# Optimization experiments

Hardware: AMD Instinct MI355X
Metric: run time of the kernel (lower is better)

Reference implementation:

```python
import jax, jax.numpy as jnp
import numpy as np

B, S, L, D, C_ENC, H = 8, 4096, 77, 1280, 2048, 20
DH = D // H          # 64
SCALE = DH ** -0.5


def setup_inputs() -> dict:
    key = jax.random.key(0)
    ks = jax.random.split(key, 8)
    return {
        "hidden_states": jax.random.normal(ks[0], (B, S, D), jnp.float32),
        "encoder_hidden_states": jax.random.normal(ks[1], (B, L, C_ENC), jnp.float32),
        "region_state": jax.random.uniform(ks[2], (B, S, L), jnp.float32),
        "Wq": jax.random.normal(ks[3], (D, D), jnp.float32) * 0.02,
        "Wk": jax.random.normal(ks[4], (C_ENC, D), jnp.float32) * 0.02,
        "Wv": jax.random.normal(ks[5], (C_ENC, D), jnp.float32) * 0.02,
        "Wo": jax.random.normal(ks[6], (D, D), jnp.float32) * 0.02,
        "bo": jnp.zeros((D,), jnp.float32),
        "sigma": jnp.ones((1,), jnp.float32) * 14.6,
    }


def reference(hidden_states, encoder_hidden_states, region_state, Wq, Wk, Wv, Wo, bo, sigma):
    # QKV projections (dense GEMMs)
    q = (hidden_states @ Wq).reshape(B, S, H, DH)            # [B,S,H,dh]
    k = (encoder_hidden_states @ Wk).reshape(B, L, H, DH)    # [B,L,H,dh]
    v = (encoder_hidden_states @ Wv).reshape(B, L, H, DH)
    # scaled attention scores (baddbmm with beta=0 == plain scaled matmul)
    scores = jnp.einsum('bshd,blhd->bhsl', q, k) * SCALE      # [B,H,S,L]
    # region-prompt bias: weight_func(w, sigma, qk) = w * log(1 + 0.1*sigma) * qk.max()
    # repeat_interleave over heads == broadcast over the head axis
    bias = region_state * (jnp.log1p(sigma[0] * 0.1) * scores.max())  # [B,S,L]
    scores = scores + bias[:, None, :, :]
    probs = jax.nn.softmax(scores, axis=-1)
    out = jnp.einsum('bhsl,blhd->bshd', probs, v).reshape(B, S, D)
    # output projection (to_out[0]); to_out[1] is dropout (identity at eval)
    return out @ Wo + bo
```

## Files before the change

### kernel.cpp

```cpp
#include <hip/hip_runtime.h>
#include <hip/hip_bf16.h>
#include <math.h>

#define NB 8
#define NS 4096
#define NL 77
#define NLP 80
#define NLPV 96
#define ND 1280
#define NC 2048
#define NH 20
#define NDH 64
#define QK_SCALE 0.125f

typedef __attribute__((ext_vector_type(4))) float f32x4;
typedef __attribute__((ext_vector_type(8))) short bf16x8;

static __device__ __forceinline__ void gload_lds16(const void* g, void* l) {
  __builtin_amdgcn_global_load_lds(
      (const __attribute__((address_space(1))) void*)g,
      (__attribute__((address_space(3))) void*)l, 16, 0, 0);
}

#define BAR() do { asm volatile("" ::: "memory"); __builtin_amdgcn_s_barrier(); asm volatile("" ::: "memory"); } while (0)
#define LGKM0() asm volatile("s_waitcnt lgkmcnt(0)" ::: "memory")

__global__ void cvt_bf16_kern(const float* __restrict__ in,
                              __hip_bfloat16* __restrict__ out, long n)
{
  long i = ((long)blockIdx.x * blockDim.x + threadIdx.x) * 4;
  long stride = (long)gridDim.x * blockDim.x * 4;
  for (; i < n; i += stride) {
    float4 v = *reinterpret_cast<const float4*>(in + i);
    union { __hip_bfloat16 h[4]; ushort4 u; } r;
    r.h[0] = __float2bfloat16(v.x);
    r.h[1] = __float2bfloat16(v.y);
    r.h[2] = __float2bfloat16(v.z);
    r.h[3] = __float2bfloat16(v.w);
    *reinterpret_cast<ushort4*>(out + i) = r.u;
  }
}

__global__ void transpose_bf16_kern(const float* __restrict__ in,
                                    __hip_bfloat16* __restrict__ out,
                                    int rows, int cols)
{
  __shared__ float t[32][33];
  int c0 = blockIdx.x * 32, r0 = blockIdx.y * 32;
  int tx = threadIdx.x, ty = threadIdx.y;
  for (int i = ty; i < 32; i += 8) {
    int r = r0 + i, c = c0 + tx;
    t[i][tx] = (r < rows && c < cols) ? in[(long)r * cols + c] : 0.f;
  }
  __syncthreads();
  for (int i = ty; i < 32; i += 8) {
    int oc = c0 + i, orr = r0 + tx;
    if (oc < cols && orr < rows)
      out[(long)oc * rows + orr] = __float2bfloat16(t[tx][i]);
  }
}

__global__ __launch_bounds__(256)
void gemm_bt_kern(const __hip_bfloat16* __restrict__ A,
                  const __hip_bfloat16* __restrict__ Bt,
                  void* __restrict__ C, const float* __restrict__ bias,
                  int M, int N, int K, int mode)
{
  __shared__ __align__(16) __hip_bfloat16 As[128 * 32];
  __shared__ __align__(16) __hip_bfloat16 Bs[128 * 32];
  const int t = threadIdx.x;
  const int lane = t & 63;
  const int w = t >> 6;
  const int wm = w >> 1, wn = w & 1;
  const int lr = lane & 15, hi = lane >> 4, lk = hi * 8;
  const long m0 = (long)blockIdx.x * 128;
  const long n0 = (long)blockIdx.y * 128;

  f32x4 acc[4][4];
#pragma unroll
  for (int mi = 0; mi < 4; ++mi)
#pragma unroll
    for (int ni = 0; ni < 4; ++ni) acc[mi][ni] = {0.f, 0.f, 0.f, 0.f};

  for (int k0 = 0; k0 < K; k0 += 32) {
    __syncthreads();
#pragma unroll
    for (int rnd = 0; rnd < 2; ++rnd) {
      int idx = rnd * 256 + t;
      int row = idx >> 2, kpp = (idx & 3) * 8;
      long arow = m0 + row; if (arow >= M) arow = M - 1;
      gload_lds16(A + arow * K + k0 + kpp, (void*)(As + idx * 8));
      long brow = n0 + row;
      gload_lds16(Bt + brow * K + k0 + kpp, (void*)(Bs + idx * 8));
    }
    __syncthreads();

    bf16x8 af[4], bfr[4];
#pragma unroll
    for (int i = 0; i < 4; ++i) {
      af[i]  = *reinterpret_cast<const bf16x8*>(As + (wm * 64 + i * 16 + lr) * 32 + lk);
      bfr[i] = *reinterpret_cast<const bf16x8*>(Bs + (wn * 64 + i * 16 + lr) * 32 + lk);
    }
#pragma unroll
    for (int mi = 0; mi < 4; ++mi)
#pragma unroll
      for (int ni = 0; ni < 4; ++ni)
        acc[mi][ni] = __builtin_amdgcn_mfma_f32_16x16x32_bf16(af[mi], bfr[ni], acc[mi][ni], 0, 0, 0);
  }

#pragma unroll
  for (int mi = 0; mi < 4; ++mi) {
#pragma unroll
    for (int r = 0; r < 4; ++r) {
      long row = m0 + wm * 64 + mi * 16 + hi * 4 + r;
      if (row < M) {
#pragma unroll
        for (int ni = 0; ni < 4; ++ni) {
          long col = n0 + wn * 64 + ni * 16 + lr;
          if (mode == 0)
            ((__hip_bfloat16*)C)[row * N + col] = __float2bfloat16(acc[mi][ni][r]);
          else
            ((float*)C)[row * N + col] = acc[mi][ni][r] + bias[col];
        }
      }
    }
  }
}

__global__ __launch_bounds__(512, 1)
void gemm256_kern(const __hip_bfloat16* __restrict__ A,
                  const __hip_bfloat16* __restrict__ Bt,
                  void* __restrict__ C, const float* __restrict__ bias,
                  int M, int N, int K, int mode)
{
  __shared__ __align__(16) __hip_bfloat16 sm[65536];
  char* smc = (char*)sm;

  const int t = threadIdx.x, lane = t & 63, w = t >> 6;
  const int wm = w >> 2, wn = w & 3;
  const int lr = lane & 15, hi = lane >> 4;

  int nwg = gridDim.x;
  int cpx = nwg >> 3;
  int swz = (blockIdx.x & 7) * cpx + (blockIdx.x >> 3);
  int nxt = N >> 8;
  int mt = swz / nxt, ntile = swz - mt * nxt;
  const long m0 = (long)mt * 256, n0 = (long)ntile * 256;

  const int rA   = w * 16 + (lane >> 3);
  const int sg8  = (((lane & 7) ^ (lane >> 3))) * 8;
  const int dst0 = (w * 128 + lane) * 8;

  const int swz16 = (hi * 16) ^ ((lr & 7) << 4);
  const int aoff0 = (wm * 128 + lr) * 128 + swz16;
  const int boff0 = (wn * 64 + lr) * 128 + swz16;

  f32x4 acc[8][4];
#pragma unroll
  for (int j = 0; j < 8; ++j)
#pragma unroll
    for (int ni = 0; ni < 4; ++ni) acc[j][ni] = {0.f, 0.f, 0.f, 0.f};

  bf16x8 af[4][2], bfr[4][2];

  auto stageA = [&](int b, int h, int kt) {
#pragma unroll
    for (int c = 0; c < 2; ++c)
      gload_lds16(A + (m0 + h * 128 + rA + c * 8) * (long)K + kt * 64 + sg8,
                  (void*)(sm + b * 16384 + h * 8192 + dst0 + c * 512));
  };
  auto stageB = [&](int b, int h, int kt) {
#pragma unroll
    for (int c = 0; c < 2; ++c)
      gload_lds16(Bt + (n0 + h * 128 + rA + c * 8) * (long)K + kt * 64 + sg8,
                  (void*)(sm + 32768 + b * 16384 + h * 8192 + dst0 + c * 512));
  };

  const int NT = K >> 6;
  stageB(0, 0, 0); stageB(0, 1, 0); stageA(0, 0, 0); stageA(0, 1, 0);
  stageB(1, 0, 1); stageB(1, 1, 1); stageA(1, 0, 1); stageA(1, 1, 1);
  asm volatile("s_waitcnt vmcnt(8)" ::: "memory");
  BAR();

  for (int t2 = 0; t2 < NT; ++t2) {
    const int b = t2 & 1;
    const char* pa = smc + b * 32768;
    const char* pb = smc + 65536 + b * 32768;
    const bool pf = (t2 + 2 < NT);

#pragma unroll
    for (int mi = 0; mi < 4; ++mi) {
      af[mi][0] = *reinterpret_cast<const bf16x8*>(pa + (aoff0 + mi * 2048));
      af[mi][1] = *reinterpret_cast<const bf16x8*>(pa + ((aoff0 ^ 64) + mi * 2048));
    }
#pragma unroll
    for (int ni = 0; ni < 2; ++ni) {
      bfr[ni][0] = *reinterpret_cast<const bf16x8*>(pb + (boff0 + ni * 2048));
      bfr[ni][1] = *reinterpret_cast<const bf16x8*>(pb + ((boff0 ^ 64) + ni * 2048));
    }
    BAR();
    LGKM0();
    __builtin_amdgcn_s_setprio(1);
#pragma unroll
    for (int mi = 0; mi < 4; ++mi)
#pragma unroll
      for (int ni = 0; ni < 2; ++ni) {
        acc[mi][ni] = __builtin_amdgcn_mfma_f32_16x16x32_bf16(af[mi][0], bfr[ni][0], acc[mi][ni], 0, 0, 0);
        acc[mi][ni] = __builtin_amdgcn_mfma_f32_16x16x32_bf16(af[mi][1], bfr[ni][1], acc[mi][ni], 0, 0, 0);
      }
    __builtin_amdgcn_s_setprio(0);
    BAR();

#pragma unroll
    for (int ni = 2; ni < 4; ++ni) {
      bfr[ni][0] = *reinterpret_cast<const bf16x8*>(pb + (boff0 + ni * 2048));
      bfr[ni][1] = *reinterpret_cast<const bf16x8*>(pb + ((boff0 ^ 64) + ni * 2048));
    }
    BAR();
    LGKM0();
    __builtin_amdgcn_s_setprio(1);
#pragma unroll
    for (int mi = 0; mi < 4; ++mi)
#pragma unroll
      for (int ni = 2; ni < 4; ++ni) {
        acc[mi][ni] = __builtin_amdgcn_mfma_f32_16x16x32_bf16(af[mi][0], bfr[ni][0], acc[mi][ni], 0, 0, 0);
        acc[mi][ni] = __builtin_amdgcn_mfma_f32_16x16x32_bf16(af[mi][1], bfr[ni][1], acc[mi][ni], 0, 0, 0);
      }
    __builtin_amdgcn_s_setprio(0);
    BAR();

#pragma unroll
    for (int mi = 0; mi < 4; ++mi) {
      af[mi][0] = *reinterpret_cast<const bf16x8*>(pa + (aoff0 + 8192 + mi * 2048));
      af[mi][1] = *reinterpret_cast<const bf16x8*>(pa + ((aoff0 ^ 64) + 8192 + mi * 2048));
    }
    if (pf) { stageB(b, 0, t2 + 2); stageB(b, 1, t2 + 2); }
    BAR();
    LGKM0();
    __builtin_amdgcn_s_setprio(1);
#pragma unroll
    for (int mi = 0; mi < 4; ++mi)
#pragma unroll
      for (int ni = 2; ni < 4; ++ni) {
        acc[mi + 4][ni] = __builtin_amdgcn_mfma_f32_16x16x32_bf16(af[mi][0], bfr[ni][0], acc[mi + 4][ni], 0, 0, 0);
        acc[mi + 4][ni] = __builtin_amdgcn_mfma_f32_16x16x32_bf16(af[mi][1], bfr[ni][1], acc[mi + 4][ni], 0, 0, 0);
      }
    __builtin_amdgcn_s_setprio(0);
    BAR();

    if (pf) { stageA(b, 0, t2 + 2); stageA(b, 1, t2 + 2); }
    BAR();
    __builtin_amdgcn_s_setprio(1);
#pragma unroll
    for (int mi = 0; mi < 4; ++mi)
#pragma unroll
      for (int ni = 0; ni < 2; ++ni) {
        acc[mi + 4][ni] = __builtin_amdgcn_mfma_f32_16x16x32_bf16(af[mi][0], bfr[ni][0], acc[mi + 4][ni], 0, 0, 0);
        acc[mi + 4][ni] = __builtin_amdgcn_mfma_f32_16x16x32_bf16(af[mi][1], bfr[ni][1], acc[mi + 4][ni], 0, 0, 0);
      }
    __builtin_amdgcn_s_setprio(0);
    if (pf) { asm volatile("s_waitcnt vmcnt(8)" ::: "memory"); }
    else    { asm volatile("s_waitcnt vmcnt(0)" ::: "memory"); }
    BAR();
  }

#pragma unroll
  for (int j = 0; j < 8; ++j) {
#pragma unroll
    for (int r = 0; r < 4; ++r) {
      long row = m0 + wm * 128 + j * 16 + hi * 4 + r;
#pragma unroll
      for (int ni = 0; ni < 4; ++ni) {
        long col = n0 + wn * 64 + ni * 16 + lr;
        if (mode == 0)
          ((__hip_bfloat16*)C)[row * N + col] = __float2bfloat16(acc[j][ni][r]);
        else
          ((float*)C)[row * N + col] = acc[j][ni][r] + bias[col];
      }
    }
  }
}

__global__ void repack_kv_kern(const __hip_bfloat16* __restrict__ kvc,
                               __hip_bfloat16* __restrict__ kp,
                               __hip_bfloat16* __restrict__ vt)
{
  int idx = blockIdx.x * 256 + threadIdx.x;
  const __hip_bfloat16 z = __float2bfloat16(0.f);
  if (idx < NB * NLP * ND) {
    int d = idx % ND;
    int l = (idx / ND) % NLP;
    int b = idx / (ND * NLP);
    kp[idx] = (l < NL) ? kvc[((long)(b * NL + l)) * 2560 + d] : z;
  }
  if (idx < NB * NH * NDH * NLPV) {
    int l  = idx % NLPV;
    int dh = (idx / NLPV) % NDH;
    int h  = (idx / (NLPV * NDH)) % NH;
    int b  = idx / (NLPV * NDH * NH);
    vt[idx] = (l < NL) ? kvc[((long)(b * NL + l)) * 2560 + ND + h * NDH + dh] : z;
  }
}

__global__ __launch_bounds__(256)
void qk_max_kern(const __hip_bfloat16* __restrict__ qb,
                 const __hip_bfloat16* __restrict__ kp,
                 float* __restrict__ bmax)
{
  int t = threadIdx.x, lane = t & 63, wi = t >> 6;
  int b = blockIdx.z, h = blockIdx.y;
  int s0 = blockIdx.x * 64 + wi * 16;
  int lr = lane & 15, lk = (lane >> 4) * 8;

  const __hip_bfloat16* Qp = qb + ((long)(b * NS + s0 + lr)) * ND + h * NDH + lk;
  bf16x8 aq0 = *reinterpret_cast<const bf16x8*>(Qp);
  bf16x8 aq1 = *reinterpret_cast<const bf16x8*>(Qp + 32);

  float m = -1e30f;
#pragma unroll
  for (int lt = 0; lt < 5; ++lt) {
    const __hip_bfloat16* Kr = kp + ((long)(b * NLP + lt * 16 + lr)) * ND + h * NDH + lk;
    bf16x8 bk0 = *reinterpret_cast<const bf16x8*>(Kr);
    bf16x8 bk1 = *reinterpret_cast<const bf16x8*>(Kr + 32);
    f32x4 sc = {0.f, 0.f, 0.f, 0.f};
    sc = __builtin_amdgcn_mfma_f32_16x16x32_bf16(aq0, bk0, sc, 0, 0, 0);
    sc = __builtin_amdgcn_mfma_f32_16x16x32_bf16(aq1, bk1, sc, 0, 0, 0);
    bool valid = (lt < 4) || (lr < 13);
    if (valid) {
#pragma unroll
      for (int r = 0; r < 4; ++r) m = fmaxf(m, sc[r]);
    }
  }
#pragma unroll
  for (int k = 32; k >= 1; k >>= 1) m = fmaxf(m, __shfl_xor(m, k));

  __shared__ float wmx[4];
  if (lane == 0) wmx[wi] = m;
  __syncthreads();
  if (t == 0) {
    float mm = fmaxf(fmaxf(wmx[0], wmx[1]), fmaxf(wmx[2], wmx[3]));
    long bid = ((long)blockIdx.z * gridDim.y + blockIdx.y) * gridDim.x + blockIdx.x;
    bmax[bid] = mm * QK_SCALE;
  }
}

__global__ void reduce_max_kern(const float* __restrict__ bm, int n,
                                const float* __restrict__ sigma,
                                float* __restrict__ cb)
{
  __shared__ float sm[256];
  float m = -1e30f;
  for (int i = threadIdx.x; i < n; i += 256) m = fmaxf(m, bm[i]);
  sm[threadIdx.x] = m;
  __syncthreads();
  for (int s = 128; s > 0; s >>= 1) {
    if (threadIdx.x < (unsigned)s) sm[threadIdx.x] = fmaxf(sm[threadIdx.x], sm[threadIdx.x + s]);
    __syncthreads();
  }
  if (threadIdx.x == 0) cb[0] = log1pf(sigma[0] * 0.1f) * sm[0];
}

__global__ __launch_bounds__(256)
void attn_kern(const __hip_bfloat16* __restrict__ qb,
               const __hip_bfloat16* __restrict__ kp,
               const __hip_bfloat16* __restrict__ vt,
               const float* __restrict__ rs,
               const float* __restrict__ cb,
               __hip_bfloat16* __restrict__ ao_out)
{
  __shared__ __align__(16) __hip_bfloat16 pl[4][16][NLPV];
  int t = threadIdx.x, lane = t & 63, wi = t >> 6;
  int b = blockIdx.z, h = blockIdx.y;
  int s0 = blockIdx.x * 64 + wi * 16;
  int lr = lane & 15, hi = lane >> 4, lk = hi * 8;
  const float c = cb[0];

  const __hip_bfloat16* Qp = qb + ((long)(b * NS + s0 + lr)) * ND + h * NDH + lk;
  bf16x8 aq0 = *reinterpret_cast<const bf16x8*>(Qp);
  bf16x8 aq1 = *reinterpret_cast<const bf16x8*>(Qp + 32);

  f32x4 sc[5];
#pragma unroll
  for (int lt = 0; lt < 5; ++lt) {
    const __hip_bfloat16* Kr = kp + ((long)(b * NLP + lt * 16 + lr)) * ND + h * NDH + lk;
    bf16x8 bk0 = *reinterpret_cast<const bf16x8*>(Kr);
    bf16x8 bk1 = *reinterpret_cast<const bf16x8*>(Kr + 32);
    f32x4 z = {0.f, 0.f, 0.f, 0.f};
    z = __builtin_amdgcn_mfma_f32_16x16x32_bf16(aq0, bk0, z, 0, 0, 0);
    sc[lt] = __builtin_amdgcn_mfma_f32_16x16x32_bf16(aq1, bk1, z, 0, 0, 0);
  }

  float sv[5][4];
  float pm[4] = {-1e30f, -1e30f, -1e30f, -1e30f};
#pragma unroll
  for (int lt = 0; lt < 5; ++lt) {
    int l = lt * 16 + lr;
#pragma unroll
    for (int r = 0; r < 4; ++r) {
      if (l < NL) {
        int srow = s0 + hi * 4 + r;
        float v = sc[lt][r] * QK_SCALE + rs[((long)(b * NS + srow)) * NL + l] * c;
        sv[lt][r] = v;
        pm[r] = fmaxf(pm[r], v);
      } else {
        sv[lt][r] = -1e30f;
      }
    }
  }
#pragma unroll
  for (int r = 0; r < 4; ++r)
#pragma unroll
    for (int k = 8; k >= 1; k >>= 1) pm[r] = fmaxf(pm[r], __shfl_xor(pm[r], k));

  float p[5][4];
  float psum[4] = {0.f, 0.f, 0.f, 0.f};
#pragma unroll
  for (int lt = 0; lt < 5; ++lt) {
    int l = lt * 16 + lr;
#pragma unroll
    for (int r = 0; r < 4; ++r) {
      float e = (l < NL) ? __expf(sv[lt][r] - pm[r]) : 0.f;
      p[lt][r] = e;
      psum[r] += e;
    }
  }
#pragma unroll
  for (int r = 0; r < 4; ++r)
#pragma unroll
    for (int k = 8; k >= 1; k >>= 1) psum[r] += __shfl_xor(psum[r], k);
  float rinv[4];
#pragma unroll
  for (int r = 0; r < 4; ++r) rinv[r] = 1.f / psum[r];

#pragma unroll
  for (int lt = 0; lt < 5; ++lt)
#pragma unroll
    for (int r = 0; r < 4; ++r)
      pl[wi][hi * 4 + r][lt * 16 + lr] = __float2bfloat16(p[lt][r]);
#pragma unroll
  for (int r = 0; r < 4; ++r)
    pl[wi][hi * 4 + r][80 + lr] = __float2bfloat16(0.f);

  f32x4 ao[4];
#pragma unroll
  for (int nt = 0; nt < 4; ++nt) ao[nt] = {0.f, 0.f, 0.f, 0.f};
  const __hip_bfloat16* Vb = vt + ((long)((b * NH + h) * NDH)) * NLPV;
#pragma unroll
  for (int ks = 0; ks < 3; ++ks) {
    bf16x8 pa = *reinterpret_cast<const bf16x8*>(&pl[wi][lr][ks * 32 + lk]);
#pragma unroll
    for (int nt = 0; nt < 4; ++nt) {
      bf16x8 bv = *reinterpret_cast<const bf16x8*>(Vb + ((long)(nt * 16 + lr)) * NLPV + ks * 32 + lk);
      ao[nt] = __builtin_amdgcn_mfma_f32_16x16x32_bf16(pa, bv, ao[nt], 0, 0, 0);
    }
  }

#pragma unroll
  for (int nt = 0; nt < 4; ++nt)
#pragma unroll
    for (int r = 0; r < 4; ++r) {
      int srow = s0 + hi * 4 + r;
      ao_out[((long)(b * NS + srow)) * ND + h * NDH + nt * 16 + lr] =
          __float2bfloat16(ao[nt][r] * rinv[r]);
    }
}

extern "C" void kernel_launch(void* const* d_in, const int* in_sizes, int n_in,
                              void* d_out, int out_size, void* d_ws, size_t ws_size,
                              hipStream_t stream)
{
  const float* hs    = (const float*)d_in[0];
  const float* ehs   = (const float*)d_in[1];
  const float* rs    = (const float*)d_in[2];
  const float* Wq    = (const float*)d_in[3];
  const float* Wk    = (const float*)d_in[4];
  const float* Wv    = (const float*)d_in[5];
  const float* Wo    = (const float*)d_in[6];
  const float* bo    = (const float*)d_in[7];
  const float* sigma = (const float*)d_in[8];
  float* out = (float*)d_out;

  char* ws = (char*)d_ws;
  size_t off = 0;
  auto alloc = [&](size_t bytes) {
    void* p = ws + off;
    off = (off + bytes + 255) & ~(size_t)255;
    return p;
  };
  __hip_bfloat16* hsb  = (__hip_bfloat16*)alloc((size_t)NB * NS * ND * 2);
  __hip_bfloat16* qb   = (__hip_bfloat16*)alloc((size_t)NB * NS * ND * 2);
  __hip_bfloat16* wqt  = (__hip_bfloat16*)alloc((size_t)ND * ND * 2);
  __hip_bfloat16* wkvt = (__hip_bfloat16*)alloc((size_t)2560 * NC * 2);
  __hip_bfloat16* wot  = (__hip_bfloat16*)alloc((size_t)ND * ND * 2);
  __hip_bfloat16* ehsb = (__hip_bfloat16*)alloc((size_t)NB * NL * NC * 2);
  __hip_bfloat16* kvc  = (__hip_bfloat16*)alloc((size_t)NB * NL * 2560 * 2);
  __hip_bfloat16* kp   = (__hip_bfloat16*)alloc((size_t)NB * NLP * ND * 2);
  __hip_bfloat16* vt   = (__hip_bfloat16*)alloc((size_t)NB * NH * NDH * NLPV * 2);
  float* bmax = (float*)alloc(10240 * 4);
  float* cb   = (float*)alloc(256);

  cvt_bf16_kern<<<2048, 256, 0, stream>>>(hs, hsb, (long)NB * NS * ND);
  cvt_bf16_kern<<<512, 256, 0, stream>>>(ehs, ehsb, (long)NB * NL * NC);

  transpose_bf16_kern<<<dim3(40, 40), dim3(32, 8), 0, stream>>>(Wq, wqt, ND, ND);
  transpose_bf16_kern<<<dim3(40, 64), dim3(32, 8), 0, stream>>>(Wk, wkvt, NC, ND);
  transpose_bf16_kern<<<dim3(40, 64), dim3(32, 8), 0, stream>>>(Wv, wkvt + (size_t)ND * NC, NC, ND);
  transpose_bf16_kern<<<dim3(40, 40), dim3(32, 8), 0, stream>>>(Wo, wot, ND, ND);

  gemm256_kern<<<640, 512, 0, stream>>>(hsb, wqt, qb, nullptr, NB * NS, ND, ND, 0);

  gemm_bt_kern<<<dim3(5, 20), 256, 0, stream>>>(ehsb, wkvt, kvc, nullptr, NB * NL, 2560, NC, 0);

  repack_kv_kern<<<3840, 256, 0, stream>>>(kvc, kp, vt);

  qk_max_kern<<<dim3(64, NH, NB), 256, 0, stream>>>(qb, kp, bmax);
  reduce_max_kern<<<1, 256, 0, stream>>>(bmax, 64 * NH * NB, sigma, cb);

  attn_kern<<<dim3(64, NH, NB), 256, 0, stream>>>(qb, kp, vt, rs, cb, hsb);

  gemm256_kern<<<640, 512, 0, stream>>>(hsb, wot, out, bo, NB * NS, ND, ND, 1);
}
```

Baseline: 581.2 us.

## Collapse GEMM main-loop barriers and stage epilogue stores through LDS

The GEMM main loop drops most intra-iteration barriers and lgkmcnt waits. It loads all four B fragments at once and issues both the A and B prefetch stages together after a single barrier. The epilogue now writes each 16-row accumulator slab into a per-wave LDS scratch area, then emits 16-byte coalesced global stores instead of scattered scalar stores. Fewer barriers should improve MFMA issue density. The risks are more register pressure, since all B fragments stay live, and LDS races: scratch and prefetch writes may overlap buffers that other waves are still reading without a barrier.

```diff
diff --git a/kernel.cpp b/kernel.cpp
--- a/kernel.cpp
+++ b/kernel.cpp
@@ -23,7 +23,6 @@
 }
 
 #define BAR() do { asm volatile("" ::: "memory"); __builtin_amdgcn_s_barrier(); asm volatile("" ::: "memory"); } while (0)
-#define LGKM0() asm volatile("s_waitcnt lgkmcnt(0)" ::: "memory")
 
 __global__ void cvt_bf16_kern(const float* __restrict__ in,
                               __hip_bfloat16* __restrict__ out, long n)
@@ -194,49 +193,25 @@
       af[mi][1] = *reinterpret_cast<const bf16x8*>(pa + ((aoff0 ^ 64) + mi * 2048));
     }
 #pragma unroll
-    for (int ni = 0; ni < 2; ++ni) {
+    for (int ni = 0; ni < 4; ++ni) {
       bfr[ni][0] = *reinterpret_cast<const bf16x8*>(pb + (boff0 + ni * 2048));
       bfr[ni][1] = *reinterpret_cast<const bf16x8*>(pb + ((boff0 ^ 64) + ni * 2048));
     }
-    BAR();
-    LGKM0();
     __builtin_amdgcn_s_setprio(1);
 #pragma unroll
     for (int mi = 0; mi < 4; ++mi)
 #pragma unroll
-      for (int ni = 0; ni < 2; ++ni) {
+      for (int ni = 0; ni < 4; ++ni) {
         acc[mi][ni] = __builtin_amdgcn_mfma_f32_16x16x32_bf16(af[mi][0], bfr[ni][0], acc[mi][ni], 0, 0, 0);
         acc[mi][ni] = __builtin_amdgcn_mfma_f32_16x16x32_bf16(af[mi][1], bfr[ni][1], acc[mi][ni], 0, 0, 0);
       }
     __builtin_amdgcn_s_setprio(0);
-    BAR();
-
-#pragma unroll
-    for (int ni = 2; ni < 4; ++ni) {
-      bfr[ni][0] = *reinterpret_cast<const bf16x8*>(pb + (boff0 + ni * 2048));
-      bfr[ni][1] = *reinterpret_cast<const bf16x8*>(pb + ((boff0 ^ 64) + ni * 2048));
-    }
-    BAR();
-    LGKM0();
-    __builtin_amdgcn_s_setprio(1);
-#pragma unroll
-    for (int mi = 0; mi < 4; ++mi)
-#pragma unroll
-      for (int ni = 2; ni < 4; ++ni) {
-        acc[mi][ni] = __builtin_amdgcn_mfma_f32_16x16x32_bf16(af[mi][0], bfr[ni][0], acc[mi][ni], 0, 0, 0);
-        acc[mi][ni] = __builtin_amdgcn_mfma_f32_16x16x32_bf16(af[mi][1], bfr[ni][1], acc[mi][ni], 0, 0, 0);
-      }
-    __builtin_amdgcn_s_setprio(0);
-    BAR();
 
 #pragma unroll
     for (int mi = 0; mi < 4; ++mi) {
       af[mi][0] = *reinterpret_cast<const bf16x8*>(pa + (aoff0 + 8192 + mi * 2048));
       af[mi][1] = *reinterpret_cast<const bf16x8*>(pa + ((aoff0 ^ 64) + 8192 + mi * 2048));
     }
-    if (pf) { stageB(b, 0, t2 + 2); stageB(b, 1, t2 + 2); }
-    BAR();
-    LGKM0();
     __builtin_amdgcn_s_setprio(1);
 #pragma unroll
     for (int mi = 0; mi < 4; ++mi)
@@ -246,10 +221,11 @@
         acc[mi + 4][ni] = __builtin_amdgcn_mfma_f32_16x16x32_bf16(af[mi][1], bfr[ni][1], acc[mi + 4][ni], 0, 0, 0);
       }
     __builtin_amdgcn_s_setprio(0);
+
     BAR();
-
-    if (pf) { stageA(b, 0, t2 + 2); stageA(b, 1, t2 + 2); }
-    BAR();
+    if (pf) { stageB(b, 0, t2 + 2); stageB(b, 1, t2 + 2);
+              stageA(b, 0, t2 + 2); stageA(b, 1, t2 + 2); }
+
     __builtin_amdgcn_s_setprio(1);
 #pragma unroll
     for (int mi = 0; mi < 4; ++mi)
@@ -259,23 +235,54 @@
         acc[mi + 4][ni] = __builtin_amdgcn_mfma_f32_16x16x32_bf16(af[mi][1], bfr[ni][1], acc[mi + 4][ni], 0, 0, 0);
       }
     __builtin_amdgcn_s_setprio(0);
+
     if (pf) { asm volatile("s_waitcnt vmcnt(8)" ::: "memory"); }
     else    { asm volatile("s_waitcnt vmcnt(0)" ::: "memory"); }
     BAR();
   }
 
-#pragma unroll
-  for (int j = 0; j < 8; ++j) {
-#pragma unroll
-    for (int r = 0; r < 4; ++r) {
-      long row = m0 + wm * 128 + j * 16 + hi * 4 + r;
-#pragma unroll
-      for (int ni = 0; ni < 4; ++ni) {
-        long col = n0 + wn * 64 + ni * 16 + lr;
-        if (mode == 0)
-          ((__hip_bfloat16*)C)[row * N + col] = __float2bfloat16(acc[j][ni][r]);
-        else
-          ((float*)C)[row * N + col] = acc[j][ni][r] + bias[col];
+  char* wsc = smc + w * 4096;
+  if (mode == 0) {
+    __hip_bfloat16* wsb = (__hip_bfloat16*)wsc;
+#pragma unroll
+    for (int j = 0; j < 8; ++j) {
+#pragma unroll
+      for (int ni = 0; ni < 4; ++ni)
+#pragma unroll
+        for (int r = 0; r < 4; ++r)
+          wsb[(hi * 4 + r) * 64 + ni * 16 + lr] = __float2bfloat16(acc[j][ni][r]);
+      asm volatile("s_waitcnt lgkmcnt(0)" ::: "memory");
+#pragma unroll
+      for (int c = 0; c < 2; ++c) {
+        int chunk = c * 64 + lane;
+        int row = chunk >> 3, col8 = chunk & 7;
+        int4 v = *reinterpret_cast<const int4*>(wsc + chunk * 16);
+        long grow = m0 + wm * 128 + j * 16 + row;
+        long gcol = n0 + wn * 64 + col8 * 8;
+        *reinterpret_cast<int4*>((__hip_bfloat16*)C + grow * N + gcol) = v;
+      }
+    }
+  } else {
+    float bv[4];
+#pragma unroll
+    for (int ni = 0; ni < 4; ++ni) bv[ni] = bias[n0 + wn * 64 + ni * 16 + lr];
+    float* wsf = (float*)wsc;
+#pragma unroll
+    for (int j = 0; j < 8; ++j) {
+#pragma unroll
+      for (int ni = 0; ni < 4; ++ni)
+#pragma unroll
+        for (int r = 0; r < 4; ++r)
+          wsf[(hi * 4 + r) * 64 + ni * 16 + lr] = acc[j][ni][r] + bv[ni];
+      asm volatile("s_waitcnt lgkmcnt(0)" ::: "memory");
+#pragma unroll
+      for (int c = 0; c < 4; ++c) {
+        int chunk = c * 64 + lane;
+        int row = chunk >> 4, col4 = chunk & 15;
+        int4 v = *reinterpret_cast<const int4*>(wsc + chunk * 16);
+        long grow = m0 + wm * 128 + j * 16 + row;
+        long gcol = n0 + wn * 64 + col4 * 4;
+        *reinterpret_cast<int4*>((float*)C + grow * N + gcol) = v;
       }
     }
   }
```

Measured after the change: 540.4 us. 1.08x faster.

## Use 128x128 GEMM tiles and process four query tiles per attention wave

Applied to the files above, without the earlier changes.

Swaps the 256x256, 512-thread GEMM for a 128x128, 256-thread kernel with two blocks per CU and a simpler single-phase MFMA loop per k-step. The QK-max and attention kernels now load each head's K fragments into registers once per wave and loop over four 16-row query tiles, cutting their grids by four. The aim is better occupancy and load balance for the large GEMMs and less redundant K loading in attention. The trade-off is lower per-tile data reuse in the GEMM and higher register pressure in the attention kernels.

```diff
diff --git a/kernel.cpp b/kernel.cpp
--- a/kernel.cpp
+++ b/kernel.cpp
@@ -127,157 +127,124 @@
   }
 }
 
-__global__ __launch_bounds__(512, 1)
-void gemm256_kern(const __hip_bfloat16* __restrict__ A,
+__global__ __launch_bounds__(256, 2)
+void gemm128_kern(const __hip_bfloat16* __restrict__ A,
                   const __hip_bfloat16* __restrict__ Bt,
                   void* __restrict__ C, const float* __restrict__ bias,
                   int M, int N, int K, int mode)
 {
-  __shared__ __align__(16) __hip_bfloat16 sm[65536];
+  __shared__ __align__(16) __hip_bfloat16 sm[32768];
   char* smc = (char*)sm;
 
   const int t = threadIdx.x, lane = t & 63, w = t >> 6;
-  const int wm = w >> 2, wn = w & 3;
+  const int wm = w >> 1, wn = w & 1;
   const int lr = lane & 15, hi = lane >> 4;
+  const int sw = lr & 7;
 
   int nwg = gridDim.x;
   int cpx = nwg >> 3;
   int swz = (blockIdx.x & 7) * cpx + (blockIdx.x >> 3);
-  int nxt = N >> 8;
+  int nxt = N >> 7;
   int mt = swz / nxt, ntile = swz - mt * nxt;
-  const long m0 = (long)mt * 256, n0 = (long)ntile * 256;
-
-  const int rA   = w * 16 + (lane >> 3);
-  const int sg8  = (((lane & 7) ^ (lane >> 3))) * 8;
-  const int dst0 = (w * 128 + lane) * 8;
-
-  const int swz16 = (hi * 16) ^ ((lr & 7) << 4);
-  const int aoff0 = (wm * 128 + lr) * 128 + swz16;
-  const int boff0 = (wn * 64 + lr) * 128 + swz16;
-
-  f32x4 acc[8][4];
-#pragma unroll
-  for (int j = 0; j < 8; ++j)
-#pragma unroll
-    for (int ni = 0; ni < 4; ++ni) acc[j][ni] = {0.f, 0.f, 0.f, 0.f};
-
-  bf16x8 af[4][2], bfr[4][2];
-
-  auto stageA = [&](int b, int h, int kt) {
-#pragma unroll
-    for (int c = 0; c < 2; ++c)
-      gload_lds16(A + (m0 + h * 128 + rA + c * 8) * (long)K + kt * 64 + sg8,
-                  (void*)(sm + b * 16384 + h * 8192 + dst0 + c * 512));
+  const long m0 = (long)mt * 128, n0 = (long)ntile * 128;
+
+  const int srow  = t >> 3;
+  const int skoff = ((t & 7) ^ (srow & 7)) * 8;
+  const int sdst  = t * 16;
+
+  f32x4 acc[4][4];
+#pragma unroll
+  for (int mi = 0; mi < 4; ++mi)
+#pragma unroll
+    for (int ni = 0; ni < 4; ++ni) acc[mi][ni] = {0.f, 0.f, 0.f, 0.f};
+
+  auto stageA = [&](int b, int kt) {
+#pragma unroll
+    for (int c = 0; c < 4; ++c)
+      gload_lds16(A + (m0 + c * 32 + srow) * (long)K + kt * 64 + skoff,
+                  (void*)(smc + b * 16384 + c * 4096 + sdst));
   };
-  auto stageB = [&](int b, int h, int kt) {
-#pragma unroll
-    for (int c = 0; c < 2; ++c)
-      gload_lds16(Bt + (n0 + h * 128 + rA + c * 8) * (long)K + kt * 64 + sg8,
-                  (void*)(sm + 32768 + b * 16384 + h * 8192 + dst0 + c * 512));
+  auto stageB = [&](int b, int kt) {
+#pragma unroll
+    for (int c = 0; c < 4; ++c)
+      gload_lds16(Bt + (n0 + c * 32 + srow) * (long)K + kt * 64 + skoff,
+                  (void*)(smc + 32768 + b * 16384 + c * 4096 + sdst));
   };
 
   const int NT = K >> 6;
-  stageB(0, 0, 0); stageB(0, 1, 0); stageA(0, 0, 0); stageA(0, 1, 0);
-  stageB(1, 0, 1); stageB(1, 1, 1); stageA(1, 0, 1); stageA(1, 1, 1);
+  stageA(0, 0); stageB(0, 0);
+  stageA(1, 1); stageB(1, 1);
   asm volatile("s_waitcnt vmcnt(8)" ::: "memory");
   BAR();
 
   for (int t2 = 0; t2 < NT; ++t2) {
     const int b = t2 & 1;
-    const char* pa = smc + b * 32768;
-    const char* pb = smc + 65536 + b * 32768;
+    const char* pa = smc + b * 16384;
+    const char* pb = smc + 32768 + b * 16384;
     const bool pf = (t2 + 2 < NT);
 
+    bf16x8 af[4][2], bfr[4][2];
 #pragma unroll
     for (int mi = 0; mi < 4; ++mi) {
-      af[mi][0] = *reinterpret_cast<const bf16x8*>(pa + (aoff0 + mi * 2048));
-      af[mi][1] = *reinterpret_cast<const bf16x8*>(pa + ((aoff0 ^ 64) + mi * 2048));
-    }
-#pragma unroll
-    for (int ni = 0; ni < 2; ++ni) {
-      bfr[ni][0] = *reinterpret_cast<const bf16x8*>(pb + (boff0 + ni * 2048));
-      bfr[ni][1] = *reinterpret_cast<const bf16x8*>(pb + ((boff0 ^ 64) + ni * 2048));
-    }
-    BAR();
-    LGKM0();
+      int row = wm * 64 + mi * 16 + lr;
+#pragma unroll
+      for (int kk = 0; kk < 2; ++kk)
+        af[mi][kk] = *reinterpret_cast<const bf16x8*>(
+            pa + row * 128 + ((((kk * 4 + hi) ^ sw)) << 4));
+    }
+#pragma unroll
+    for (int ni = 0; ni < 4; ++ni) {
+      int row = wn * 64 + ni * 16 + lr;
+#pragma unroll
+      for (int kk = 0; kk < 2; ++kk)
+        bfr[ni][kk] = *reinterpret_cast<const bf16x8*>(
+            pb + row * 128 + ((((kk * 4 + hi) ^ sw)) << 4));
+    }
     __builtin_amdgcn_s_setprio(1);
 #pragma unroll
     for (int mi = 0; mi < 4; ++mi)
 #pragma unroll
-      for (int ni = 0; ni < 2; ++ni) {
+      for (int ni = 0; ni < 4; ++ni) {
         acc[mi][ni] = __builtin_amdgcn_mfma_f32_16x16x32_bf16(af[mi][0], bfr[ni][0], acc[mi][ni], 0, 0, 0);
         acc[mi][ni] = __builtin_amdgcn_mfma_f32_16x16x32_bf16(af[mi][1], bfr[ni][1], acc[mi][ni], 0, 0, 0);
       }
     __builtin_amdgcn_s_setprio(0);
+
+    LGKM0();
     BAR();
-
-#pragma unroll
-    for (int ni = 2; ni < 4; ++ni) {
-      bfr[ni][0] = *reinterpret_cast<const bf16x8*>(pb + (boff0 + ni * 2048));
-      bfr[ni][1] = *reinterpret_cast<const bf16x8*>(pb + ((boff0 ^ 64) + ni * 2048));
-    }
-    BAR();
-    LGKM0();
-    __builtin_amdgcn_s_setprio(1);
-#pragma unroll
-    for (int mi = 0; mi < 4; ++mi)
-#pragma unroll
-      for (int ni = 2; ni < 4; ++ni) {
-        acc[mi][ni] = __builtin_amdgcn_mfma_f32_16x16x32_bf16(af[mi][0], bfr[ni][0], acc[mi][ni], 0, 0, 0);
-        acc[mi][ni] = __builtin_amdgcn_mfma_f32_16x16x32_bf16(af[mi][1], bfr[ni][1], acc[mi][ni], 0, 0, 0);
-      }
-    __builtin_amdgcn_s_setprio(0);
-    BAR();
-
-#pragma unroll
-    for (int mi = 0; mi < 4; ++mi) {
-      af[mi][0] = *reinterpret_cast<const bf16x8*>(pa + (aoff0 + 8192 + mi * 2048));
-      af[mi][1] = *reinterpret_cast<const bf16x8*>(pa + ((aoff0 ^ 64) + 8192 + mi * 2048));
-    }
-    if (pf) { stageB(b, 0, t2 + 2); stageB(b, 1, t2 + 2); }
-    BAR();
-    LGKM0();
-    __builtin_amdgcn_s_setprio(1);
-#pragma unroll
-    for (int mi = 0; mi < 4; ++mi)
-#pragma unroll
-      for (int ni = 2; ni < 4; ++ni) {
-        acc[mi + 4][ni] = __builtin_amdgcn_mfma_f32_16x16x32_bf16(af[mi][0], bfr[ni][0], acc[mi + 4][ni], 0, 0, 0);
-        acc[mi + 4][ni] = __builtin_amdgcn_mfma_f32_16x16x32_bf16(af[mi][1], bfr[ni][1], acc[mi + 4][ni], 0, 0, 0);
-      }
-    __builtin_amdgcn_s_setprio(0);
-    BAR();
-
-    if (pf) { stageA(b, 0, t2 + 2); stageA(b, 1, t2 + 2); }
-    BAR();
-    __builtin_amdgcn_s_setprio(1);
-#pragma unroll
-    for (int mi = 0; mi < 4; ++mi)
-#pragma unroll
-      for (int ni = 0; ni < 2; ++ni) {
-        acc[mi + 4][ni] = __builtin_amdgcn_mfma_f32_16x16x32_bf16(af[mi][0], bfr[ni][0], acc[mi + 4][ni], 0, 0, 0);
-        acc[mi + 4][ni] = __builtin_amdgcn_mfma_f32_16x16x32_bf16(af[mi][1], bfr[ni][1], acc[mi + 4][ni], 0, 0, 0);
-      }
-    __builtin_amdgcn_s_setprio(0);
+    if (pf) { stageA(b, t2 + 2); stageB(b, t2 + 2); }
     if (pf) { asm volatile("s_waitcnt vmcnt(8)" ::: "memory"); }
     else    { asm volatile("s_waitcnt vmcnt(0)" ::: "memory"); }
     BAR();
   }
 
-#pragma unroll
-  for (int j = 0; j < 8; ++j) {
-#pragma unroll
-    for (int r = 0; r < 4; ++r) {
-      long row = m0 + wm * 128 + j * 16 + hi * 4 + r;
-#pragma unroll
-      for (int ni = 0; ni < 4; ++ni) {
-        long col = n0 + wn * 64 + ni * 16 + lr;
-        if (mode == 0)
-          ((__hip_bfloat16*)C)[row * N + col] = __float2bfloat16(acc[j][ni][r]);
-        else
-          ((float*)C)[row * N + col] = acc[j][ni][r] + bias[col];
-      }
-    }
+  if (mode == 0) {
+#pragma unroll
+    for (int mi = 0; mi < 4; ++mi)
+#pragma unroll
+      for (int r = 0; r < 4; ++r) {
+        long row = m0 + wm * 64 + mi * 16 + hi * 4 + r;
+#pragma unroll
+        for (int ni = 0; ni < 4; ++ni) {
+          long col = n0 + wn * 64 + ni * 16 + lr;
+          ((__hip_bfloat16*)C)[row * N + col] = __float2bfloat16(acc[mi][ni][r]);
+        }
+      }
+  } else {
+    float bv[4];
+#pragma unroll
+    for (int ni = 0; ni < 4; ++ni) bv[ni] = bias[n0 + wn * 64 + ni * 16 + lr];
+#pragma unroll
+    for (int mi = 0; mi < 4; ++mi)
+#pragma unroll
+      for (int r = 0; r < 4; ++r) {
+        long row = m0 + wm * 64 + mi * 16 + hi * 4 + r;
+#pragma unroll
+        for (int ni = 0; ni < 4; ++ni) {
+          long col = n0 + wn * 64 + ni * 16 + lr;
+          ((float*)C)[row * N + col] = acc[mi][ni][r] + bv[ni];
+        }
+      }
   }
 }
 
@@ -309,26 +276,33 @@
 {
   int t = threadIdx.x, lane = t & 63, wi = t >> 6;
   int b = blockIdx.z, h = blockIdx.y;
-  int s0 = blockIdx.x * 64 + wi * 16;
   int lr = lane & 15, lk = (lane >> 4) * 8;
 
-  const __hip_bfloat16* Qp = qb + ((long)(b * NS + s0 + lr)) * ND + h * NDH + lk;
-  bf16x8 aq0 = *reinterpret_cast<const bf16x8*>(Qp);
-  bf16x8 aq1 = *reinterpret_cast<const bf16x8*>(Qp + 32);
-
-  float m = -1e30f;
+  bf16x8 bk[5][2];
 #pragma unroll
   for (int lt = 0; lt < 5; ++lt) {
     const __hip_bfloat16* Kr = kp + ((long)(b * NLP + lt * 16 + lr)) * ND + h * NDH + lk;
-    bf16x8 bk0 = *reinterpret_cast<const bf16x8*>(Kr);
-    bf16x8 bk1 = *reinterpret_cast<const bf16x8*>(Kr + 32);
-    f32x4 sc = {0.f, 0.f, 0.f, 0.f};
-    sc = __builtin_amdgcn_mfma_f32_16x16x32_bf16(aq0, bk0, sc, 0, 0, 0);
-    sc = __builtin_amdgcn_mfma_f32_16x16x32_bf16(aq1, bk1, sc, 0, 0, 0);
-    bool valid = (lt < 4) || (lr < 13);
-    if (valid) {
-#pragma unroll
-      for (int r = 0; r < 4; ++r) m = fmaxf(m, sc[r]);
+    bk[lt][0] = *reinterpret_cast<const bf16x8*>(Kr);
+    bk[lt][1] = *reinterpret_cast<const bf16x8*>(Kr + 32);
+  }
+
+  float m = -1e30f;
+#pragma unroll
+  for (int st = 0; st < 4; ++st) {
+    int s0 = blockIdx.x * 256 + wi * 64 + st * 16;
+    const __hip_bfloat16* Qp = qb + ((long)(b * NS + s0 + lr)) * ND + h * NDH + lk;
+    bf16x8 aq0 = *reinterpret_cast<const bf16x8*>(Qp);
+    bf16x8 aq1 = *reinterpret_cast<const bf16x8*>(Qp + 32);
+#pragma unroll
+    for (int lt = 0; lt < 5; ++lt) {
+      f32x4 sc = {0.f, 0.f, 0.f, 0.f};
+      sc = __builtin_amdgcn_mfma_f32_16x16x32_bf16(aq0, bk[lt][0], sc, 0, 0, 0);
+      sc = __builtin_amdgcn_mfma_f32_16x16x32_bf16(aq1, bk[lt][1], sc, 0, 0, 0);
+      bool valid = (lt < 4) || (lr < 13);
+      if (valid) {
+#pragma unroll
+        for (int r = 0; r < 4; ++r) m = fmaxf(m, sc[r]);
+      }
     }
   }
 #pragma unroll
@@ -371,98 +345,111 @@
   __shared__ __align__(16) __hip_bfloat16 pl[4][16][NLPV];
   int t = threadIdx.x, lane = t & 63, wi = t >> 6;
   int b = blockIdx.z, h = blockIdx.y;
-  int s0 = blockIdx.x * 64 + wi * 16;
   int lr = lane & 15, hi = lane >> 4, lk = hi * 8;
   const float c = cb[0];
 
-  const __hip_bfloat16* Qp = qb + ((long)(b * NS + s0 + lr)) * ND + h * NDH + lk;
-  bf16x8 aq0 = *reinterpret_cast<const bf16x8*>(Qp);
-  bf16x8 aq1 = *reinterpret_cast<const bf16x8*>(Qp + 32);
-
-  f32x4 sc[5];
+  bf16x8 bk[5][2];
 #pragma unroll
   for (int lt = 0; lt < 5; ++lt) {
     const __hip_bfloat16* Kr = kp + ((long)(b * NLP + lt * 16 + lr)) * ND + h * NDH + lk;
-    bf16x8 bk0 = *reinterpret_cast<const bf16x8*>(Kr);
-    bf16x8 bk1 = *reinterpret_cast<const bf16x8*>(Kr + 32);
-    f32x4 z = {0.f, 0.f, 0.f, 0.f};
-    z = __builtin_amdgcn_mfma_f32_16x16x32_bf16(aq0, bk0, z, 0, 0, 0);
-    sc[lt] = __builtin_amdgcn_mfma_f32_16x16x32_bf16(aq1, bk1, z, 0, 0, 0);
-  }
-
-  float sv[5][4];
-  float pm[4] = {-1e30f, -1e30f, -1e30f, -1e30f};
-#pragma unroll
-  for (int lt = 0; lt < 5; ++lt) {
-    int l = lt * 16 + lr;
-#pragma unroll
-    for (int r = 0; r < 4; ++r) {
-      if (l < NL) {
-        int srow = s0 + hi * 4 + r;
-        float v = sc[lt][r] * QK_SCALE + rs[((long)(b * NS + srow)) * NL + l] * c;
-        sv[lt][r] = v;
-        pm[r] = fmaxf(pm[r], v);
-      } else {
-        sv[lt][r] = -1e30f;
-      }
-    }
-  }
-#pragma unroll
-  for (int r = 0; r < 4; ++r)
-#pragma unroll
-    for (int k = 8; k >= 1; k >>= 1) pm[r] = fmaxf(pm[r], __shfl_xor(pm[r], k));
-
-  float p[5][4];
-  float psum[4] = {0.f, 0.f, 0.f, 0.f};
-#pragma unroll
-  for (int lt = 0; lt < 5; ++lt) {
-    int l = lt * 16 + lr;
-#pragma unroll
-    for (int r = 0; r < 4; ++r) {
-      float e = (l < NL) ? __expf(sv[lt][r] - pm[r]) : 0.f;
-      p[lt][r] = e;
-      psum[r] += e;
-    }
-  }
-#pragma unroll
-  for (int r = 0; r < 4; ++r)
-#pragma unroll
-    for (int k = 8; k >= 1; k >>= 1) psum[r] += __shfl_xor(psum[r], k);
-  float rinv[4];
-#pragma unroll
-  for (int r = 0; r < 4; ++r) rinv[r] = 1.f / psum[r];
-
-#pragma unroll
-  for (int lt = 0; lt < 5; ++lt)
-#pragma unroll
-    for (int r = 0; r < 4; ++r)
-      pl[wi][hi * 4 + r][lt * 16 + lr] = __float2bfloat16(p[lt][r]);
+    bk[lt][0] = *reinterpret_cast<const bf16x8*>(Kr);
+    bk[lt][1] = *reinterpret_cast<const bf16x8*>(Kr + 32);
+  }
 #pragma unroll
   for (int r = 0; r < 4; ++r)
     pl[wi][hi * 4 + r][80 + lr] = __float2bfloat16(0.f);
 
-  f32x4 ao[4];
-#pragma unroll
-  for (int nt = 0; nt < 4; ++nt) ao[nt] = {0.f, 0.f, 0.f, 0.f};
   const __hip_bfloat16* Vb = vt + ((long)((b * NH + h) * NDH)) * NLPV;
-#pragma unroll
-  for (int ks = 0; ks < 3; ++ks) {
-    bf16x8 pa = *reinterpret_cast<const bf16x8*>(&pl[wi][lr][ks * 32 + lk]);
-#pragma unroll
-    for (int nt = 0; nt < 4; ++nt) {
-      bf16x8 bv = *reinterpret_cast<const bf16x8*>(Vb + ((long)(nt * 16 + lr)) * NLPV + ks * 32 + lk);
-      ao[nt] = __builtin_amdgcn_mfma_f32_16x16x32_bf16(pa, bv, ao[nt], 0, 0, 0);
-    }
-  }
-
-#pragma unroll
-  for (int nt = 0; nt < 4; ++nt)
-#pragma unroll
-    for (int r = 0; r < 4; ++r) {
-      int srow = s0 + hi * 4 + r;
-      ao_out[((long)(b * NS + srow)) * ND + h * NDH + nt * 16 + lr] =
-          __float2bfloat16(ao[nt][r] * rinv[r]);
-    }
+
+#pragma unroll
+  for (int st = 0; st < 4; ++st) {
+    int s0 = blockIdx.x * 256 + wi * 64 + st * 16;
+    const __hip_bfloat16* Qp = qb + ((long)(b * NS + s0 + lr)) * ND + h * NDH + lk;
+    bf16x8 aq0 = *reinterpret_cast<const bf16x8*>(Qp);
+    bf16x8 aq1 = *reinterpret_cast<const bf16x8*>(Qp + 32);
+
+    f32x4 sc[5];
+#pragma unroll
+    for (int lt = 0; lt < 5; ++lt) {
+      f32x4 z = {0.f, 0.f, 0.f, 0.f};
+      z = __builtin_amdgcn_mfma_f32_16x16x32_bf16(aq0, bk[lt][0], z, 0, 0, 0);
+      sc[lt] = __builtin_amdgcn_mfma_f32_16x16x32_bf16(aq1, bk[lt][1], z, 0, 0, 0);
+    }
+
+    float sv[5][4];
+    float pm[4] = {-1e30f, -1e30f, -1e30f, -1e30f};
+#pragma unroll
+    for (int lt = 0; lt < 5; ++lt) {
+      int l = lt * 16 + lr;
+#pragma unroll
+      for (int r = 0; r < 4; ++r) {
+        if (l < NL) {
+          int srow = s0 + hi * 4 + r;
+          float v = sc[lt][r] * QK_SCALE + rs[((long)(b * NS + srow)) * NL + l] * c;
+          sv[lt][r] = v;
+          pm[r] = fmaxf(pm[r], v);
+        } else {
+          sv[lt][r] = -1e30f;
+        }
+      }
+    }
+#pragma unroll
+    for (int r = 0; r < 4; ++r)
+#pragma unroll
+      for (int k = 8; k >= 1; k >>= 1) pm[r] = fmaxf(pm[r], __shfl_xor(pm[r], k));
+
+    float p[5][4];
+    float psum[4] = {0.f, 0.f, 0.f, 0.f};
+#pragma unroll
+    for (int lt = 0; lt < 5; ++lt) {
+      int l = lt * 16 + lr;
+#pragma unroll
+      for (int r = 0; r < 4; ++r) {
+        float e = (l < NL) ? __expf(sv[lt][r] - pm[r]) : 0.f;
+        p[lt][r] = e;
+        psum[r] += e;
+      }
+    }
+#pragma unroll
+    for (int r = 0; r < 4; ++r)
+#pragma unroll
+      for (int k = 8; k >= 1; k >>= 1) psum[r] += __shfl_xor(psum[r], k);
+    float rinv[4];
+#pragma unroll
+    for (int r = 0; r < 4; ++r) rinv[r] = 1.f / psum[r];
+
+    LGKM0();
+
+#pragma unroll
+    for (int lt = 0; lt < 5; ++lt)
+#pragma unroll
+      for (int r = 0; r < 4; ++r)
+        pl[wi][hi * 4 + r][lt * 16 + lr] = __float2bfloat16(p[lt][r]);
+
+    LGKM0();
+
+    f32x4 ao[4];
+#pragma unroll
+    for (int nt = 0; nt < 4; ++nt) ao[nt] = {0.f, 0.f, 0.f, 0.f};
+#pragma unroll
+    for (int ks = 0; ks < 3; ++ks) {
+      bf16x8 pa = *reinterpret_cast<const bf16x8*>(&pl[wi][lr][ks * 32 + lk]);
+#pragma unroll
+      for (int nt = 0; nt < 4; ++nt) {
+        bf16x8 bv = *reinterpret_cast<const bf16x8*>(Vb + ((long)(nt * 16 + lr)) * NLPV + ks * 32 + lk);
+        ao[nt] = __builtin_amdgcn_mfma_f32_16x16x32_bf16(pa, bv, ao[nt], 0, 0, 0);
+      }
+    }
+
+#pragma unroll
+    for (int nt = 0; nt < 4; ++nt)
+#pragma unroll
+      for (int r = 0; r < 4; ++r) {
+        int srow = s0 + hi * 4 + r;
+        ao_out[((long)(b * NS + srow)) * ND + h * NDH + nt * 16 + lr] =
+            __float2bfloat16(ao[nt][r] * rinv[r]);
+      }
+  }
 }
 
 extern "C" void kernel_launch(void* const* d_in, const int* in_sizes, int n_in,
@@ -507,16 +494,16 @@
   transpose_bf16_kern<<<dim3(40, 64), dim3(32, 8), 0, stream>>>(Wv, wkvt + (size_t)ND * NC, NC, ND);
   transpose_bf16_kern<<<dim3(40, 40), dim3(32, 8), 0, stream>>>(Wo, wot, ND, ND);
 
-  gemm256_kern<<<640, 512, 0, stream>>>(hsb, wqt, qb, nullptr, NB * NS, ND, ND, 0);
+  gemm128_kern<<<2560, 256, 0, stream>>>(hsb, wqt, qb, nullptr, NB * NS, ND, ND, 0);
 
   gemm_bt_kern<<<dim3(5, 20), 256, 0, stream>>>(ehsb, wkvt, kvc, nullptr, NB * NL, 2560, NC, 0);
 
   repack_kv_kern<<<3840, 256, 0, stream>>>(kvc, kp, vt);
 
-  qk_max_kern<<<dim3(64, NH, NB), 256, 0, stream>>>(qb, kp, bmax);
-  reduce_max_kern<<<1, 256, 0, stream>>>(bmax, 64 * NH * NB, sigma, cb);
-
-  attn_kern<<<dim3(64, NH, NB), 256, 0, stream>>>(qb, kp, vt, rs, cb, hsb);
-
-  gemm256_kern<<<640, 512, 0, stream>>>(hsb, wot, out, bo, NB * NS, ND, ND, 1);
-}
+  qk_max_kern<<<dim3(16, NH, NB), 256, 0, stream>>>(qb, kp, bmax);
+  reduce_max_kern<<<1, 256, 0, stream>>>(bmax, 16 * NH * NB, sigma, cb);
+
+  attn_kern<<<dim3(16, NH, NB), 256, 0, stream>>>(qb, kp, vt, rs, cb, hsb);
+
+  gemm128_kern<<<2560, 256, 0, stream>>>(hsb, wot, out, bo, NB * NS, ND, ND, 1);
+}
```

Result: faster. 502.5 us (-13.6%).
